# Kernel optimization log

Measured on AMD Instinct MI355X. Metric: run time of the kernel, lower is better.

The kernel has to match this reference:

```python
import jax, jax.numpy as jnp
import numpy as np
import math

B, H, S, D = 2, 16, 2048, 128

def setup_inputs() -> dict:
    key = jax.random.key(0)
    k1, k2, k3, k4 = jax.random.split(key, 4)
    x1 = jax.random.normal(k1, (B, H, S, D), dtype=jnp.float32)
    x2 = jax.random.normal(k2, (B, H, S, D), dtype=jnp.float32)
    x3 = jax.random.normal(k3, (B, H, D, S), dtype=jnp.float32)
    attn_mask = jax.random.normal(k4, (S, S), dtype=jnp.float32)
    return {"x1": x1, "x2": x2, "x3": x3, "attn_mask": attn_mask}

def reference(x1, x2, x3, attn_mask):
    scale = 1.0 / math.sqrt(x1.shape[-1])
    # [B,H,S,S] scores
    qk = jnp.einsum('bhqd,bhkd->bhqk', x1, x2) * scale + attn_mask
    attn_weight = jax.nn.softmax(qk, axis=-1)
    # x3 @ attn_weight : [B,H,D,S] @ [B,H,S,S] -> [B,H,D,S]
    output = jnp.einsum('bhds,bhsk->bhdk', x3, attn_weight)
    return output
```

## Files before the change

kernel.cpp:

```cpp
#include <hip/hip_runtime.h>


typedef __attribute__((ext_vector_type(8))) short short8;
typedef __attribute__((ext_vector_type(4))) float f32x4;

#define S_LEN 2048
#define D_LEN 128
#define BH_N 32
#define SCALE_QK 0.08838834764831845f

__device__ __forceinline__ unsigned short f2bf(float f) {
    union { float f; unsigned int i; } v; v.f = f;
    unsigned int r = v.i + 0x7FFFu + ((v.i >> 16) & 1u);
    return (unsigned short)(r >> 16);
}
__device__ __forceinline__ float bf2f(unsigned short u) {
    union { unsigned int i; float f; } v; v.i = ((unsigned int)u) << 16; return v.f;
}
__device__ __forceinline__ uint2 pack4bf(float4 v) {
    uint2 p;
    p.x = (unsigned)f2bf(v.x) | ((unsigned)f2bf(v.y) << 16);
    p.y = (unsigned)f2bf(v.z) | ((unsigned)f2bf(v.w) << 16);
    return p;
}

__global__ void k_cvt(const float* __restrict__ x1,
                      const float* __restrict__ x2,
                      const float* __restrict__ mask,
                      unsigned short* __restrict__ x1s,
                      unsigned short* __restrict__ x2b,
                      unsigned short* __restrict__ mbf) {
    const size_t N1 = (size_t)BH_N * S_LEN * D_LEN;
    const size_t NM = (size_t)S_LEN * S_LEN;
    size_t i = ((size_t)blockIdx.x * 256 + threadIdx.x) * 4;
    if (i < N1) {
        float4 v = *(const float4*)&x1[i];
        v.x *= SCALE_QK; v.y *= SCALE_QK; v.z *= SCALE_QK; v.w *= SCALE_QK;
        *(uint2*)&x1s[i] = pack4bf(v);
    } else if (i < 2 * N1) {
        size_t j = i - N1;
        float4 v = *(const float4*)&x2[j];
        *(uint2*)&x2b[j] = pack4bf(v);
    } else if (i < 2 * N1 + NM) {
        size_t j = i - 2 * N1;
        float4 v = *(const float4*)&mask[j];
        *(uint2*)&mbf[j] = pack4bf(v);
    }
}

__global__ __launch_bounds__(256, 3) void k_qk(
    const unsigned short* __restrict__ x1s,
    const unsigned short* __restrict__ x2b,
    const unsigned short* __restrict__ mbf,
    const float* __restrict__ x3,
    unsigned short* __restrict__ x3s)
{
    __shared__ unsigned short sQ[128 * 136];
    __shared__ unsigned short sK[64 * 136];
    __shared__ float sRL[128];
    const int q0 = blockIdx.x * 128;
    const int bh = blockIdx.y;
    const unsigned short* x1p = x1s + (size_t)bh * S_LEN * D_LEN;
    const unsigned short* x2p = x2b + (size_t)bh * S_LEN * D_LEN;
    const int t = threadIdx.x;
    const int w = t >> 6, lane = t & 63, quad = lane >> 4, l16 = lane & 15;

#pragma unroll
    for (int i = 0; i < 8; ++i) {
        int e = (i * 256 + t) * 8;
        int r = e >> 7, c = e & 127;
        *(uint4*)&sQ[r * 136 + c] = *(const uint4*)&x1p[(size_t)(q0 + r) * D_LEN + c];
    }

    float rs[8] = {0.f, 0.f, 0.f, 0.f, 0.f, 0.f, 0.f, 0.f};

    for (int k0 = 0; k0 < S_LEN; k0 += 64) {
        __syncthreads();
#pragma unroll
        for (int i = 0; i < 4; ++i) {
            int e = (i * 256 + t) * 8;
            int r = e >> 7, c = e & 127;
            *(uint4*)&sK[r * 136 + c] = *(const uint4*)&x2p[(size_t)(k0 + r) * D_LEN + c];
        }
        __syncthreads();

        f32x4 acc[2][4];
#pragma unroll
        for (int qb = 0; qb < 2; ++qb)
#pragma unroll
            for (int kb = 0; kb < 4; ++kb) acc[qb][kb] = (f32x4){0.f, 0.f, 0.f, 0.f};
#pragma unroll
        for (int kk = 0; kk < 4; ++kk) {
            short8 a0 = *(const short8*)&sQ[(32 * w + l16) * 136 + kk * 32 + quad * 8];
            short8 a1 = *(const short8*)&sQ[(32 * w + 16 + l16) * 136 + kk * 32 + quad * 8];
            short8 b[4];
#pragma unroll
            for (int kb = 0; kb < 4; ++kb)
                b[kb] = *(const short8*)&sK[(kb * 16 + l16) * 136 + kk * 32 + quad * 8];
#pragma unroll
            for (int kb = 0; kb < 4; ++kb) {
                acc[0][kb] = __builtin_amdgcn_mfma_f32_16x16x32_bf16(a0, b[kb], acc[0][kb], 0, 0, 0);
                acc[1][kb] = __builtin_amdgcn_mfma_f32_16x16x32_bf16(a1, b[kb], acc[1][kb], 0, 0, 0);
            }
        }
#pragma unroll
        for (int qb = 0; qb < 2; ++qb) {
            const int qrow = 32 * w + 16 * qb + 4 * quad;
#pragma unroll
            for (int kb = 0; kb < 4; ++kb) {
                const int kg = k0 + kb * 16 + l16;
#pragma unroll
                for (int r = 0; r < 4; ++r) {
                    float m = bf2f(mbf[(size_t)(q0 + qrow + r) * S_LEN + kg]);
                    rs[qb * 4 + r] += __expf(acc[qb][kb][r] + m);
                }
            }
        }
    }
#pragma unroll
    for (int i = 0; i < 8; ++i) {
        float v = rs[i];
        v += __shfl_xor(v, 1);
        v += __shfl_xor(v, 2);
        v += __shfl_xor(v, 4);
        v += __shfl_xor(v, 8);
        if (l16 == 0) sRL[32 * w + 16 * (i >> 2) + 4 * quad + (i & 3)] = 1.0f / v;
    }
    __syncthreads();

    const float* x3b = x3 + (size_t)bh * (size_t)D_LEN * S_LEN;
    unsigned short* x3sp = x3s + (size_t)bh * (size_t)D_LEN * S_LEN;
#pragma unroll
    for (int i = 0; i < 16; ++i) {
        int e = (i * 256 + t) * 4;
        int r = e >> 7, c = e & 127;
        float4 v = *(const float4*)&x3b[(size_t)r * S_LEN + q0 + c];
        v.x *= sRL[c]; v.y *= sRL[c + 1]; v.z *= sRL[c + 2]; v.w *= sRL[c + 3];
        *(uint2*)&x3sp[(size_t)r * S_LEN + q0 + c] = pack4bf(v);
    }
}

__global__ __launch_bounds__(256, 2) void k_out(
    const unsigned short* __restrict__ x1s,
    const unsigned short* __restrict__ x2b,
    const unsigned short* __restrict__ x3s,
    const unsigned short* __restrict__ mbf,
    float* __restrict__ out)
{
    __shared__ unsigned short sK[64 * 136];
    __shared__ unsigned short sQ[64 * 136];
    __shared__ unsigned short sX[128 * 72];
    __shared__ unsigned short sE[64 * 72];
    const int kb0 = blockIdx.x * 64;
    const int bh = blockIdx.y;
    const unsigned short* x1p = x1s + (size_t)bh * S_LEN * D_LEN;
    const unsigned short* x2p = x2b + (size_t)bh * S_LEN * D_LEN;
    const unsigned short* x3p = x3s + (size_t)bh * (size_t)D_LEN * S_LEN;
    const int t = threadIdx.x;
    const int w = t >> 6, lane = t & 63, quad = lane >> 4, l16 = lane & 15;

#pragma unroll
    for (int i = 0; i < 4; ++i) {
        int e = (i * 256 + t) * 8;
        int r = e >> 7, c = e & 127;
        *(uint4*)&sK[r * 136 + c] = *(const uint4*)&x2p[(size_t)(kb0 + r) * D_LEN + c];
    }

    f32x4 oa[8];
#pragma unroll
    for (int i = 0; i < 8; ++i) oa[i] = (f32x4){0.f, 0.f, 0.f, 0.f};

    for (int q0 = 0; q0 < S_LEN; q0 += 64) {
        __syncthreads();
#pragma unroll
        for (int i = 0; i < 4; ++i) {
            int e = (i * 256 + t) * 8;
            int r = e >> 7, c = e & 127;
            *(uint4*)&sQ[r * 136 + c] = *(const uint4*)&x1p[(size_t)(q0 + r) * D_LEN + c];
        }
#pragma unroll
        for (int i = 0; i < 4; ++i) {
            int e = (i * 256 + t) * 8;
            int r = e >> 6, c = e & 63;
            *(uint4*)&sX[r * 72 + c] = *(const uint4*)&x3p[(size_t)r * S_LEN + q0 + c];
        }
        __syncthreads();

        f32x4 acc[4];
#pragma unroll
        for (int kb = 0; kb < 4; ++kb) acc[kb] = (f32x4){0.f, 0.f, 0.f, 0.f};
#pragma unroll
        for (int kk = 0; kk < 4; ++kk) {
            short8 a = *(const short8*)&sQ[(16 * w + l16) * 136 + kk * 32 + quad * 8];
            short8 b[4];
#pragma unroll
            for (int kb = 0; kb < 4; ++kb)
                b[kb] = *(const short8*)&sK[(kb * 16 + l16) * 136 + kk * 32 + quad * 8];
#pragma unroll
            for (int kb = 0; kb < 4; ++kb)
                acc[kb] = __builtin_amdgcn_mfma_f32_16x16x32_bf16(a, b[kb], acc[kb], 0, 0, 0);
        }
        const int qrow = 16 * w + 4 * quad;
#pragma unroll
        for (int kb = 0; kb < 4; ++kb) {
            const int kg = kb0 + kb * 16 + l16;
            unsigned short e4[4];
#pragma unroll
            for (int r = 0; r < 4; ++r) {
                float m = bf2f(mbf[(size_t)(q0 + qrow + r) * S_LEN + kg]);
                e4[r] = f2bf(__expf(acc[kb][r] + m));
            }
            uint2 pk;
            pk.x = (unsigned)e4[0] | ((unsigned)e4[1] << 16);
            pk.y = (unsigned)e4[2] | ((unsigned)e4[3] << 16);
            *(uint2*)&sE[(kb * 16 + l16) * 72 + qrow] = pk;
        }
        __syncthreads();

#pragma unroll
        for (int kk = 0; kk < 2; ++kk) {
            short8 a[2];
#pragma unroll
            for (int db = 0; db < 2; ++db)
                a[db] = *(const short8*)&sX[(32 * w + 16 * db + l16) * 72 + kk * 32 + quad * 8];
            short8 b[4];
#pragma unroll
            for (int kb = 0; kb < 4; ++kb)
                b[kb] = *(const short8*)&sE[(kb * 16 + l16) * 72 + kk * 32 + quad * 8];
#pragma unroll
            for (int db = 0; db < 2; ++db)
#pragma unroll
                for (int kb = 0; kb < 4; ++kb)
                    oa[db * 4 + kb] = __builtin_amdgcn_mfma_f32_16x16x32_bf16(a[db], b[kb], oa[db * 4 + kb], 0, 0, 0);
        }
    }

#pragma unroll
    for (int db = 0; db < 2; ++db)
#pragma unroll
        for (int kb = 0; kb < 4; ++kb)
#pragma unroll
            for (int r = 0; r < 4; ++r) {
                int d = 32 * w + 16 * db + 4 * quad + r;
                out[((size_t)bh * D_LEN + d) * S_LEN + kb0 + kb * 16 + l16] =
                    oa[db * 4 + kb][r];
            }
}

__global__ __launch_bounds__(256, 3) void k_rowsum_fb(
    const float* __restrict__ x1, const float* __restrict__ x2,
    const float* __restrict__ mask, float* __restrict__ rl)
{
    __shared__ unsigned short sQ[128 * 136];
    __shared__ unsigned short sK[64 * 136];
    const int q0 = blockIdx.x * 128;
    const int bh = blockIdx.y;
    const float* x1b = x1 + (size_t)bh * S_LEN * D_LEN;
    const float* x2b = x2 + (size_t)bh * S_LEN * D_LEN;
    const int t = threadIdx.x;
    const int w = t >> 6, lane = t & 63, quad = lane >> 4, l16 = lane & 15;
#pragma unroll
    for (int i = 0; i < 16; ++i) {
        int e = (i * 256 + t) * 4;
        int r = e >> 7, c = e & 127;
        float4 v = *(const float4*)&x1b[(size_t)(q0 + r) * D_LEN + c];
        *(uint2*)&sQ[r * 136 + c] = pack4bf(v);
    }
    float rs[8] = {0.f, 0.f, 0.f, 0.f, 0.f, 0.f, 0.f, 0.f};
    for (int k0 = 0; k0 < S_LEN; k0 += 64) {
        __syncthreads();
#pragma unroll
        for (int i = 0; i < 8; ++i) {
            int e = (i * 256 + t) * 4;
            int r = e >> 7, c = e & 127;
            float4 v = *(const float4*)&x2b[(size_t)(k0 + r) * D_LEN + c];
            *(uint2*)&sK[r * 136 + c] = pack4bf(v);
        }
        __syncthreads();
#pragma unroll
        for (int qb = 0; qb < 2; ++qb) {
            const int qrow = 32 * w + 16 * qb;
#pragma unroll
            for (int kb = 0; kb < 4; ++kb) {
                f32x4 acc = {0.f, 0.f, 0.f, 0.f};
#pragma unroll
                for (int kk = 0; kk < 4; ++kk) {
                    short8 a = *(const short8*)&sQ[(qrow + l16) * 136 + kk * 32 + quad * 8];
                    short8 b = *(const short8*)&sK[(kb * 16 + l16) * 136 + kk * 32 + quad * 8];
                    acc = __builtin_amdgcn_mfma_f32_16x16x32_bf16(a, b, acc, 0, 0, 0);
                }
                const int kg = k0 + kb * 16 + l16;
                const int qg = q0 + qrow + 4 * quad;
#pragma unroll
                for (int r = 0; r < 4; ++r) {
                    float m = mask[(size_t)(qg + r) * S_LEN + kg];
                    rs[qb * 4 + r] += __expf(acc[r] * SCALE_QK + m);
                }
            }
        }
    }
#pragma unroll
    for (int i = 0; i < 8; ++i) {
        float v = rs[i];
        v += __shfl_xor(v, 1); v += __shfl_xor(v, 2);
        v += __shfl_xor(v, 4); v += __shfl_xor(v, 8);
        if (l16 == 0) {
            int qg = q0 + 32 * w + 16 * (i >> 2) + 4 * quad + (i & 3);
            rl[(size_t)bh * S_LEN + qg] = 1.0f / v;
        }
    }
}

__global__ __launch_bounds__(256, 2) void k_out_fb(
    const float* __restrict__ x1, const float* __restrict__ x2,
    const float* __restrict__ x3, const float* __restrict__ mask,
    const float* __restrict__ rl, float* __restrict__ out)
{
    __shared__ unsigned short sK[64 * 136];
    __shared__ unsigned short sQ[64 * 136];
    __shared__ unsigned short sX[128 * 72];
    __shared__ unsigned short sE[64 * 72];
    const int kb0 = blockIdx.x * 64;
    const int bh = blockIdx.y;
    const float* x1b = x1 + (size_t)bh * S_LEN * D_LEN;
    const float* x2b = x2 + (size_t)bh * S_LEN * D_LEN;
    const float* x3b = x3 + (size_t)bh * (size_t)D_LEN * S_LEN;
    const float* rlb = rl + (size_t)bh * S_LEN;
    const int t = threadIdx.x;
    const int w = t >> 6, lane = t & 63, quad = lane >> 4, l16 = lane & 15;
#pragma unroll
    for (int i = 0; i < 8; ++i) {
        int e = (i * 256 + t) * 4;
        int r = e >> 7, c = e & 127;
        float4 v = *(const float4*)&x2b[(size_t)(kb0 + r) * D_LEN + c];
        *(uint2*)&sK[r * 136 + c] = pack4bf(v);
    }
    f32x4 oa[8];
#pragma unroll
    for (int i = 0; i < 8; ++i) oa[i] = (f32x4){0.f, 0.f, 0.f, 0.f};
    for (int q0 = 0; q0 < S_LEN; q0 += 64) {
        __syncthreads();
#pragma unroll
        for (int i = 0; i < 8; ++i) {
            int e = (i * 256 + t) * 4;
            int r = e >> 7, c = e & 127;
            float4 v = *(const float4*)&x1b[(size_t)(q0 + r) * D_LEN + c];
            *(uint2*)&sQ[r * 136 + c] = pack4bf(v);
        }
#pragma unroll
        for (int i = 0; i < 8; ++i) {
            int e = (i * 256 + t) * 4;
            int r = e >> 6, c = e & 63;
            float4 v = *(const float4*)&x3b[(size_t)r * S_LEN + q0 + c];
            *(uint2*)&sX[r * 72 + c] = pack4bf(v);
        }
        __syncthreads();
        const int qrow = 16 * w + 4 * quad;
        float rl4[4];
#pragma unroll
        for (int r = 0; r < 4; ++r) rl4[r] = rlb[q0 + qrow + r];
#pragma unroll
        for (int kb = 0; kb < 4; ++kb) {
            f32x4 acc = {0.f, 0.f, 0.f, 0.f};
#pragma unroll
            for (int kk = 0; kk < 4; ++kk) {
                short8 a = *(const short8*)&sQ[(16 * w + l16) * 136 + kk * 32 + quad * 8];
                short8 b = *(const short8*)&sK[(kb * 16 + l16) * 136 + kk * 32 + quad * 8];
                acc = __builtin_amdgcn_mfma_f32_16x16x32_bf16(a, b, acc, 0, 0, 0);
            }
            const int kg = kb0 + kb * 16 + l16;
            unsigned short e4[4];
#pragma unroll
            for (int r = 0; r < 4; ++r) {
                float m = mask[(size_t)(q0 + qrow + r) * S_LEN + kg];
                e4[r] = f2bf(__expf(acc[r] * SCALE_QK + m) * rl4[r]);
            }
            uint2 pk;
            pk.x = (unsigned)e4[0] | ((unsigned)e4[1] << 16);
            pk.y = (unsigned)e4[2] | ((unsigned)e4[3] << 16);
            *(uint2*)&sE[(kb * 16 + l16) * 72 + qrow] = pk;
        }
        __syncthreads();
#pragma unroll
        for (int db = 0; db < 2; ++db)
#pragma unroll
            for (int kb = 0; kb < 4; ++kb) {
                f32x4 a0 = oa[db * 4 + kb];
#pragma unroll
                for (int kk = 0; kk < 2; ++kk) {
                    short8 a = *(const short8*)&sX[(32 * w + 16 * db + l16) * 72 + kk * 32 + quad * 8];
                    short8 b = *(const short8*)&sE[(kb * 16 + l16) * 72 + kk * 32 + quad * 8];
                    a0 = __builtin_amdgcn_mfma_f32_16x16x32_bf16(a, b, a0, 0, 0, 0);
                }
                oa[db * 4 + kb] = a0;
            }
    }
#pragma unroll
    for (int db = 0; db < 2; ++db)
#pragma unroll
        for (int kb = 0; kb < 4; ++kb)
#pragma unroll
            for (int r = 0; r < 4; ++r) {
                int d = 32 * w + 16 * db + 4 * quad + r;
                out[((size_t)bh * D_LEN + d) * S_LEN + kb0 + kb * 16 + l16] =
                    oa[db * 4 + kb][r];
            }
}

extern "C" void kernel_launch(void* const* d_in, const int* in_sizes, int n_in,
                              void* d_out, int out_size, void* d_ws, size_t ws_size,
                              hipStream_t stream) {
    const float* x1 = (const float*)d_in[0];
    const float* x2 = (const float*)d_in[1];
    const float* x3 = (const float*)d_in[2];
    const float* mask = (const float*)d_in[3];
    float* out = (float*)d_out;

    const size_t N1 = (size_t)BH_N * S_LEN * D_LEN;
    const size_t NM = (size_t)S_LEN * S_LEN;
    const size_t need = (3 * N1 + NM) * sizeof(unsigned short);

    if (ws_size >= need) {
        unsigned short* x1s = (unsigned short*)d_ws;
        unsigned short* x2b = x1s + N1;
        unsigned short* x3s = x2b + N1;
        unsigned short* mbf = x3s + N1;
        const size_t tot4 = (2 * N1 + NM) / 4;
        k_cvt<<<dim3((unsigned)(tot4 / 256)), dim3(256), 0, stream>>>(x1, x2, mask, x1s, x2b, mbf);
        k_qk<<<dim3(S_LEN / 128, BH_N), dim3(256), 0, stream>>>(x1s, x2b, mbf, x3, x3s);
        k_out<<<dim3(S_LEN / 64, BH_N), dim3(256), 0, stream>>>(x1s, x2b, x3s, mbf, out);
    } else {
        float* rl = (float*)d_ws;
        k_rowsum_fb<<<dim3(S_LEN / 128, BH_N), dim3(256), 0, stream>>>(x1, x2, mask, rl);
        k_out_fb<<<dim3(S_LEN / 64, BH_N), dim3(256), 0, stream>>>(x1, x2, x3, mask, rl, out);
    }
}
```

Baseline: 347.2 us.

## Use XOR-swizzled LDS layouts and larger key tiles in both attention kernels

Both kernels replace padded shared-memory rows with XOR-swizzled unpadded layouts to avoid bank conflicts. k_qk now processes 128-key tiles with transposed MFMA operands, so the mask is read as contiguous 4-element vectors, and the row sums are reduced across waves through shared memory. k_out doubles its key tile to 128, halving the grid and the number of passes over Q/X3 per key, in exchange for more accumulator registers and lower occupancy.

```diff
diff --git a/kernel.cpp b/kernel.cpp
--- a/kernel.cpp
+++ b/kernel.cpp
@@ -48,15 +48,16 @@
     }
 }
 
-__global__ __launch_bounds__(256, 3) void k_qk(
+__global__ __launch_bounds__(256, 2) void k_qk(
     const unsigned short* __restrict__ x1s,
     const unsigned short* __restrict__ x2b,
     const unsigned short* __restrict__ mbf,
     const float* __restrict__ x3,
     unsigned short* __restrict__ x3s)
 {
-    __shared__ unsigned short sQ[128 * 136];
-    __shared__ unsigned short sK[64 * 136];
+    __shared__ unsigned short sQ[128 * 128];
+    __shared__ unsigned short sK[128 * 128];
+    __shared__ float sRSp[4][128];
     __shared__ float sRL[128];
     const int q0 = blockIdx.x * 128;
     const int bh = blockIdx.y;
@@ -67,64 +68,74 @@
 
 #pragma unroll
     for (int i = 0; i < 8; ++i) {
-        int e = (i * 256 + t) * 8;
-        int r = e >> 7, c = e & 127;
-        *(uint4*)&sQ[r * 136 + c] = *(const uint4*)&x1p[(size_t)(q0 + r) * D_LEN + c];
+        int idx = i * 256 + t;
+        int r = idx >> 4, c = idx & 15;
+        *(uint4*)&sQ[r * 128 + ((c ^ (r & 7)) * 8)] =
+            *(const uint4*)&x1p[(size_t)(q0 + r) * D_LEN + c * 8];
     }
 
     float rs[8] = {0.f, 0.f, 0.f, 0.f, 0.f, 0.f, 0.f, 0.f};
 
-    for (int k0 = 0; k0 < S_LEN; k0 += 64) {
-        __syncthreads();
-#pragma unroll
-        for (int i = 0; i < 4; ++i) {
-            int e = (i * 256 + t) * 8;
-            int r = e >> 7, c = e & 127;
-            *(uint4*)&sK[r * 136 + c] = *(const uint4*)&x2p[(size_t)(k0 + r) * D_LEN + c];
-        }
-        __syncthreads();
-
-        f32x4 acc[2][4];
-#pragma unroll
-        for (int qb = 0; qb < 2; ++qb)
-#pragma unroll
-            for (int kb = 0; kb < 4; ++kb) acc[qb][kb] = (f32x4){0.f, 0.f, 0.f, 0.f};
+    for (int k0 = 0; k0 < S_LEN; k0 += 128) {
+        __syncthreads();
+#pragma unroll
+        for (int i = 0; i < 8; ++i) {
+            int idx = i * 256 + t;
+            int r = idx >> 4, c = idx & 15;
+            *(uint4*)&sK[r * 128 + ((c ^ (r & 7)) * 8)] =
+                *(const uint4*)&x2p[(size_t)(k0 + r) * D_LEN + c * 8];
+        }
+        __syncthreads();
+
+        f32x4 acc[2][8];
+#pragma unroll
+        for (int kb = 0; kb < 2; ++kb)
+#pragma unroll
+            for (int qt = 0; qt < 8; ++qt) acc[kb][qt] = (f32x4){0.f, 0.f, 0.f, 0.f};
 #pragma unroll
         for (int kk = 0; kk < 4; ++kk) {
-            short8 a0 = *(const short8*)&sQ[(32 * w + l16) * 136 + kk * 32 + quad * 8];
-            short8 a1 = *(const short8*)&sQ[(32 * w + 16 + l16) * 136 + kk * 32 + quad * 8];
-            short8 b[4];
-#pragma unroll
-            for (int kb = 0; kb < 4; ++kb)
-                b[kb] = *(const short8*)&sK[(kb * 16 + l16) * 136 + kk * 32 + quad * 8];
-#pragma unroll
-            for (int kb = 0; kb < 4; ++kb) {
-                acc[0][kb] = __builtin_amdgcn_mfma_f32_16x16x32_bf16(a0, b[kb], acc[0][kb], 0, 0, 0);
-                acc[1][kb] = __builtin_amdgcn_mfma_f32_16x16x32_bf16(a1, b[kb], acc[1][kb], 0, 0, 0);
-            }
-        }
-#pragma unroll
-        for (int qb = 0; qb < 2; ++qb) {
-            const int qrow = 32 * w + 16 * qb + 4 * quad;
-#pragma unroll
-            for (int kb = 0; kb < 4; ++kb) {
-                const int kg = k0 + kb * 16 + l16;
-#pragma unroll
-                for (int r = 0; r < 4; ++r) {
-                    float m = bf2f(mbf[(size_t)(q0 + qrow + r) * S_LEN + kg]);
-                    rs[qb * 4 + r] += __expf(acc[qb][kb][r] + m);
-                }
-            }
-        }
-    }
-#pragma unroll
-    for (int i = 0; i < 8; ++i) {
-        float v = rs[i];
-        v += __shfl_xor(v, 1);
-        v += __shfl_xor(v, 2);
-        v += __shfl_xor(v, 4);
-        v += __shfl_xor(v, 8);
-        if (l16 == 0) sRL[32 * w + 16 * (i >> 2) + 4 * quad + (i & 3)] = 1.0f / v;
+            const int sc = ((kk * 4 + quad) ^ (l16 & 7)) * 8;
+            short8 a[2];
+#pragma unroll
+            for (int kb = 0; kb < 2; ++kb)
+                a[kb] = *(const short8*)&sK[(32 * w + kb * 16 + l16) * 128 + sc];
+            short8 b[8];
+#pragma unroll
+            for (int qt = 0; qt < 8; ++qt)
+                b[qt] = *(const short8*)&sQ[(qt * 16 + l16) * 128 + sc];
+#pragma unroll
+            for (int kb = 0; kb < 2; ++kb)
+#pragma unroll
+                for (int qt = 0; qt < 8; ++qt)
+                    acc[kb][qt] = __builtin_amdgcn_mfma_f32_16x16x32_bf16(a[kb], b[qt], acc[kb][qt], 0, 0, 0);
+        }
+#pragma unroll
+        for (int kb = 0; kb < 2; ++kb) {
+            const int kg = k0 + 32 * w + 16 * kb + 4 * quad;
+#pragma unroll
+            for (int qt = 0; qt < 8; ++qt) {
+                const int qg = q0 + qt * 16 + l16;
+                uint2 m2 = *(const uint2*)&mbf[(size_t)qg * S_LEN + kg];
+                float m0 = bf2f((unsigned short)(m2.x & 0xFFFF));
+                float m1 = bf2f((unsigned short)(m2.x >> 16));
+                float m2f = bf2f((unsigned short)(m2.y & 0xFFFF));
+                float m3 = bf2f((unsigned short)(m2.y >> 16));
+                rs[qt] += __expf(acc[kb][qt][0] + m0) + __expf(acc[kb][qt][1] + m1)
+                        + __expf(acc[kb][qt][2] + m2f) + __expf(acc[kb][qt][3] + m3);
+            }
+        }
+    }
+#pragma unroll
+    for (int qt = 0; qt < 8; ++qt) {
+        float v = rs[qt];
+        v += __shfl_xor(v, 16);
+        v += __shfl_xor(v, 32);
+        if (lane < 16) sRSp[w][qt * 16 + lane] = v;
+    }
+    __syncthreads();
+    if (t < 128) {
+        float tot = sRSp[0][t] + sRSp[1][t] + sRSp[2][t] + sRSp[3][t];
+        sRL[t] = 1.0f / tot;
     }
     __syncthreads();
 
@@ -147,11 +158,11 @@
     const unsigned short* __restrict__ mbf,
     float* __restrict__ out)
 {
-    __shared__ unsigned short sK[64 * 136];
-    __shared__ unsigned short sQ[64 * 136];
-    __shared__ unsigned short sX[128 * 72];
-    __shared__ unsigned short sE[64 * 72];
-    const int kb0 = blockIdx.x * 64;
+    __shared__ unsigned short sK[128 * 128];
+    __shared__ unsigned short sQ[64 * 128];
+    __shared__ unsigned short sX[128 * 64];
+    __shared__ unsigned short sE[128 * 64];
+    const int kb0 = blockIdx.x * 128;
     const int bh = blockIdx.y;
     const unsigned short* x1p = x1s + (size_t)bh * S_LEN * D_LEN;
     const unsigned short* x2p = x2b + (size_t)bh * S_LEN * D_LEN;
@@ -160,49 +171,55 @@
     const int w = t >> 6, lane = t & 63, quad = lane >> 4, l16 = lane & 15;
 
 #pragma unroll
-    for (int i = 0; i < 4; ++i) {
-        int e = (i * 256 + t) * 8;
-        int r = e >> 7, c = e & 127;
-        *(uint4*)&sK[r * 136 + c] = *(const uint4*)&x2p[(size_t)(kb0 + r) * D_LEN + c];
-    }
-
-    f32x4 oa[8];
-#pragma unroll
-    for (int i = 0; i < 8; ++i) oa[i] = (f32x4){0.f, 0.f, 0.f, 0.f};
+    for (int i = 0; i < 8; ++i) {
+        int idx = i * 256 + t;
+        int r = idx >> 4, c = idx & 15;
+        *(uint4*)&sK[r * 128 + ((c ^ (r & 7)) * 8)] =
+            *(const uint4*)&x2p[(size_t)(kb0 + r) * D_LEN + c * 8];
+    }
+
+    f32x4 oa[16];
+#pragma unroll
+    for (int i = 0; i < 16; ++i) oa[i] = (f32x4){0.f, 0.f, 0.f, 0.f};
 
     for (int q0 = 0; q0 < S_LEN; q0 += 64) {
         __syncthreads();
 #pragma unroll
         for (int i = 0; i < 4; ++i) {
-            int e = (i * 256 + t) * 8;
-            int r = e >> 7, c = e & 127;
-            *(uint4*)&sQ[r * 136 + c] = *(const uint4*)&x1p[(size_t)(q0 + r) * D_LEN + c];
+            int idx = i * 256 + t;
+            int r = idx >> 4, c = idx & 15;
+            *(uint4*)&sQ[r * 128 + ((c ^ (r & 7)) * 8)] =
+                *(const uint4*)&x1p[(size_t)(q0 + r) * D_LEN + c * 8];
         }
 #pragma unroll
         for (int i = 0; i < 4; ++i) {
-            int e = (i * 256 + t) * 8;
-            int r = e >> 6, c = e & 63;
-            *(uint4*)&sX[r * 72 + c] = *(const uint4*)&x3p[(size_t)r * S_LEN + q0 + c];
-        }
-        __syncthreads();
-
-        f32x4 acc[4];
-#pragma unroll
-        for (int kb = 0; kb < 4; ++kb) acc[kb] = (f32x4){0.f, 0.f, 0.f, 0.f};
+            int idx = i * 256 + t;
+            int r = idx >> 3, c = idx & 7;
+            *(uint4*)&sX[r * 64 + ((c ^ (r & 7)) * 8)] =
+                *(const uint4*)&x3p[(size_t)r * S_LEN + q0 + c * 8];
+        }
+        __syncthreads();
+
+        f32x4 acc[8];
+#pragma unroll
+        for (int kb = 0; kb < 8; ++kb) acc[kb] = (f32x4){0.f, 0.f, 0.f, 0.f};
 #pragma unroll
         for (int kk = 0; kk < 4; ++kk) {
-            short8 a = *(const short8*)&sQ[(16 * w + l16) * 136 + kk * 32 + quad * 8];
-            short8 b[4];
-#pragma unroll
-            for (int kb = 0; kb < 4; ++kb)
-                b[kb] = *(const short8*)&sK[(kb * 16 + l16) * 136 + kk * 32 + quad * 8];
-#pragma unroll
-            for (int kb = 0; kb < 4; ++kb)
+            const int sc = ((kk * 4 + quad) ^ (l16 & 7)) * 8;
+            short8 a = *(const short8*)&sQ[(16 * w + l16) * 128 + sc];
+            short8 b[8];
+#pragma unroll
+            for (int kb = 0; kb < 8; ++kb)
+                b[kb] = *(const short8*)&sK[(kb * 16 + l16) * 128 + sc];
+#pragma unroll
+            for (int kb = 0; kb < 8; ++kb)
                 acc[kb] = __builtin_amdgcn_mfma_f32_16x16x32_bf16(a, b[kb], acc[kb], 0, 0, 0);
         }
         const int qrow = 16 * w + 4 * quad;
-#pragma unroll
-        for (int kb = 0; kb < 4; ++kb) {
+        const int qoff7 = (16 * w + 4 * quad) & 7;
+        const int cE = (16 * w + 4 * quad) >> 3;
+#pragma unroll
+        for (int kb = 0; kb < 8; ++kb) {
             const int kg = kb0 + kb * 16 + l16;
             unsigned short e4[4];
 #pragma unroll
@@ -213,37 +230,39 @@
             uint2 pk;
             pk.x = (unsigned)e4[0] | ((unsigned)e4[1] << 16);
             pk.y = (unsigned)e4[2] | ((unsigned)e4[3] << 16);
-            *(uint2*)&sE[(kb * 16 + l16) * 72 + qrow] = pk;
+            const int krow = kb * 16 + l16;
+            *(uint2*)&sE[krow * 64 + ((cE ^ (krow & 7)) * 8) + qoff7] = pk;
         }
         __syncthreads();
 
 #pragma unroll
         for (int kk = 0; kk < 2; ++kk) {
+            const int sc = ((kk * 4 + quad) ^ (l16 & 7)) * 8;
             short8 a[2];
 #pragma unroll
             for (int db = 0; db < 2; ++db)
-                a[db] = *(const short8*)&sX[(32 * w + 16 * db + l16) * 72 + kk * 32 + quad * 8];
-            short8 b[4];
-#pragma unroll
-            for (int kb = 0; kb < 4; ++kb)
-                b[kb] = *(const short8*)&sE[(kb * 16 + l16) * 72 + kk * 32 + quad * 8];
+                a[db] = *(const short8*)&sX[(32 * w + 16 * db + l16) * 64 + sc];
+            short8 b[8];
+#pragma unroll
+            for (int kb = 0; kb < 8; ++kb)
+                b[kb] = *(const short8*)&sE[(kb * 16 + l16) * 64 + sc];
 #pragma unroll
             for (int db = 0; db < 2; ++db)
 #pragma unroll
-                for (int kb = 0; kb < 4; ++kb)
-                    oa[db * 4 + kb] = __builtin_amdgcn_mfma_f32_16x16x32_bf16(a[db], b[kb], oa[db * 4 + kb], 0, 0, 0);
+                for (int kb = 0; kb < 8; ++kb)
+                    oa[db * 8 + kb] = __builtin_amdgcn_mfma_f32_16x16x32_bf16(a[db], b[kb], oa[db * 8 + kb], 0, 0, 0);
         }
     }
 
 #pragma unroll
     for (int db = 0; db < 2; ++db)
 #pragma unroll
-        for (int kb = 0; kb < 4; ++kb)
+        for (int kb = 0; kb < 8; ++kb)
 #pragma unroll
             for (int r = 0; r < 4; ++r) {
                 int d = 32 * w + 16 * db + 4 * quad + r;
                 out[((size_t)bh * D_LEN + d) * S_LEN + kb0 + kb * 16 + l16] =
-                    oa[db * 4 + kb][r];
+                    oa[db * 8 + kb][r];
             }
 }
 
@@ -428,7 +447,7 @@
         const size_t tot4 = (2 * N1 + NM) / 4;
         k_cvt<<<dim3((unsigned)(tot4 / 256)), dim3(256), 0, stream>>>(x1, x2, mask, x1s, x2b, mbf);
         k_qk<<<dim3(S_LEN / 128, BH_N), dim3(256), 0, stream>>>(x1s, x2b, mbf, x3, x3s);
-        k_out<<<dim3(S_LEN / 64, BH_N), dim3(256), 0, stream>>>(x1s, x2b, x3s, mbf, out);
+        k_out<<<dim3(S_LEN / 128, BH_N), dim3(256), 0, stream>>>(x1s, x2b, x3s, mbf, out);
     } else {
         float* rl = (float*)d_ws;
         k_rowsum_fb<<<dim3(S_LEN / 128, BH_N), dim3(256), 0, stream>>>(x1, x2, mask, rl);
```

New measurement: 332.8 us. 1.04x faster.
